# Kernel optimization log

Measured on AMD Instinct MI355X. Metric: run time of the kernel, lower is better.

Reference implementation:

```python
import jax, jax.numpy as jnp
import numpy as np

H_IMG, W_IMG = 224, 224  # image_size default in forward


def setup_inputs() -> dict:
    key = jax.random.key(0)
    k0, k1, k2 = jax.random.split(key, 3)
    B, C, M, N = 4, 256, 1024, 16384
    xyz_feats = jax.random.normal(k0, (B, C, M), jnp.float32)
    # projections land inside the image for a realistic bin distribution
    points = jax.random.uniform(k1, (B, N, 3), jnp.float32).at[..., 2].add(0.5)
    centers = jax.random.uniform(k2, (B, M, 3), jnp.float32).at[..., 2].add(0.5)
    fx = fy = 0.5 * W_IMG  # plausible intrinsics already scaled to 224x224
    K = jnp.array([[fx, 0.0, W_IMG / 2.0],
                   [0.0, fy, H_IMG / 2.0],
                   [0.0, 0.0, 1.0]], jnp.float32)
    return {"xyz_feats": xyz_feats, "points": points, "centers": centers,
            "K": K, "kernel_size": 4}


def reference(xyz_feats, points, centers, K, kernel_size):
    B, C, M = xyz_feats.shape
    N = points.shape[1]
    H, W = H_IMG, W_IMG

    # --- interpolating_points: PointNet++ 3-NN inverse-distance interp ---
    # squared pairwise distances [B, N, M]
    d2 = (jnp.sum(points * points, -1)[:, :, None]
          + jnp.sum(centers * centers, -1)[:, None, :]
          - 2.0 * jnp.einsum('bnd,bmd->bnm', points, centers))
    neg_d, idx = jax.lax.top_k(-d2, 3)            # 3 nearest centers, [B,N,3]
    w = 1.0 / (-neg_d + 1e-8)                     # inverse-distance weights
    w = w / jnp.sum(w, -1, keepdims=True)
    b3 = jnp.arange(B)[:, None, None]
    gathered = xyz_feats[b3, :, idx]              # [B, N, 3, C]
    interp = jnp.einsum('bnkc,bnk->bnc', gathered, w)  # [B, N, C]

    # --- project_to_image ---
    uvz = jnp.einsum('ij,bnj->bni', K, points)    # [B, N, 3]
    uv = uvz[..., :2] / jnp.maximum(uvz[..., 2:], 1e-8)
    u = jnp.clip(jnp.floor(uv[..., 0]), 0, W - 1).astype(jnp.int32)
    v = jnp.clip(jnp.floor(uv[..., 1]), 0, H - 1).astype(jnp.int32)
    idx_flat = u + v * W                          # [B, N]

    # --- scatter-add binning + count normalize ---
    bb = jnp.arange(B)[:, None]
    feat_map = jnp.zeros((B, H * W, C), interp.dtype).at[bb, idx_flat].add(interp)
    count = jnp.zeros((B, H * W), interp.dtype).at[bb, idx_flat].add(1.0)
    feat_map = feat_map / jnp.maximum(count, 1.0)[..., None]
    feat_map = feat_map.reshape(B, H, W, C).transpose(0, 3, 1, 2)  # [B,C,H,W]

    # --- avg_pool2d(kernel_size, stride=kernel_size) ---
    k = kernel_size
    out = feat_map.reshape(B, C, H // k, k, W // k, k).mean(axis=(3, 5))
    return out
```

## Files before the change

kernel.cpp:

```cpp
#include <hip/hip_runtime.h>
#include <hip/hip_bf16.h>

#define H_IMG 224
#define W_IMG 224
#define B_ 4
#define C_ 256
#define M_ 1024
#define N_ 16384
#define HW_ (H_IMG * W_IMG)
#define OH_ 56
#define OW_ 56
#define NBLK_ (OH_ * OW_)
#define NBINS_ (B_ * NBLK_)
#define NT_ (B_ * N_)
#define SEG_ 32
#define MAXSEG_ (NBINS_ + NT_ / SEG_)
#define KS_ 8
#define MC_ (M_ / KS_)
#define ZTOT_ (NBINS_ * C_ + B_ * HW_ + 2 * NBINS_ + 1)

__global__ __launch_bounds__(1024) void transpose_kernel(
    const float* __restrict__ xyz, float* __restrict__ XT,
    float* __restrict__ zeroRegion)
{
    __shared__ float tile[32][33];
    int b  = blockIdx.z;
    int c0 = blockIdx.x * 32;
    int m0 = blockIdx.y * 32;
    int tx = threadIdx.x, ty = threadIdx.y;
    int flat = ((blockIdx.z * gridDim.y + blockIdx.y) * gridDim.x + blockIdx.x)
               * 1024 + ty * 32 + tx;
    for (int i = flat; i < ZTOT_; i += 1024 * 1024) zeroRegion[i] = 0.0f;
    tile[ty][tx] = xyz[(b * C_ + c0 + ty) * M_ + m0 + tx];
    __syncthreads();
    XT[(b * M_ + m0 + ty) * C_ + c0 + tx] = tile[tx][ty];
}

__global__ __launch_bounds__(1024) void top3_kernel(
    const float* __restrict__ points, const float* __restrict__ centers,
    const float* __restrict__ Kmat,
    int* __restrict__ pixA, int* __restrict__ idA, float* __restrict__ wA,
    float* __restrict__ cnt, int* __restrict__ binCnt)
{
#pragma clang fp contract(off)
    __shared__ float4 cen[M_];
    __shared__ float  pd[KS_][256][3];
    __shared__ int    pi[KS_][256][3];
    int b  = blockIdx.y;
    int t  = threadIdx.x;
    int pl = t & 127;
    int s  = t >> 7;
    int nbase = blockIdx.x * 256;

    {
        float cx = centers[(b * M_ + t) * 3 + 0];
        float cy = centers[(b * M_ + t) * 3 + 1];
        float cz = centers[(b * M_ + t) * 3 + 2];
        float c2 = ((cx * cx) + (cy * cy)) + (cz * cz);
        cen[t] = make_float4(cx, cy, cz, c2);
    }
    __syncthreads();

    int nA = b * N_ + nbase + pl;
    int nB = nA + 128;
    float pxA = points[nA * 3 + 0], pyA = points[nA * 3 + 1], pzA = points[nA * 3 + 2];
    float pxB = points[nB * 3 + 0], pyB = points[nB * 3 + 1], pzB = points[nB * 3 + 2];
    float p2A = ((pxA * pxA) + (pyA * pyA)) + (pzA * pzA);
    float p2B = ((pxB * pxB) + (pyB * pyB)) + (pzB * pzB);

    float d0a = 1e30f, d1a = 1e30f, d2a = 1e30f;
    int   i0a = 0, i1a = 0, i2a = 0;
    float d0b = 1e30f, d1b = 1e30f, d2b = 1e30f;
    int   i0b = 0, i1b = 0, i2b = 0;
    int mbase = s * MC_;
#pragma unroll 2
    for (int j = 0; j < MC_; ++j) {
        int m = mbase + j;
        float4 cc = cen[m];
        float dotA = ((pzA * cc.z) + (pyA * cc.y)) + (pxA * cc.x);
        float dA   = (p2A + cc.w) - (2.0f * dotA);
        float dotB = ((pzB * cc.z) + (pyB * cc.y)) + (pxB * cc.x);
        float dB   = (p2B + cc.w) - (2.0f * dotB);
        if (dA < d2a) {
            if (dA < d1a) {
                d2a = d1a; i2a = i1a;
                if (dA < d0a) { d1a = d0a; i1a = i0a; d0a = dA; i0a = m; }
                else          { d1a = dA;  i1a = m; }
            } else { d2a = dA; i2a = m; }
        }
        if (dB < d2b) {
            if (dB < d1b) {
                d2b = d1b; i2b = i1b;
                if (dB < d0b) { d1b = d0b; i1b = i0b; d0b = dB; i0b = m; }
                else          { d1b = dB;  i1b = m; }
            } else { d2b = dB; i2b = m; }
        }
    }
    pd[s][pl][0] = d0a;  pd[s][pl][1] = d1a;  pd[s][pl][2] = d2a;
    pi[s][pl][0] = i0a;  pi[s][pl][1] = i1a;  pi[s][pl][2] = i2a;
    pd[s][pl + 128][0] = d0b;  pd[s][pl + 128][1] = d1b;  pd[s][pl + 128][2] = d2b;
    pi[s][pl + 128][0] = i0b;  pi[s][pl + 128][1] = i1b;  pi[s][pl + 128][2] = i2b;
    __syncthreads();

    if (t < 256) {
        float md0 = 1e30f, md1 = 1e30f, md2 = 1e30f;
        int   mi0 = M_,    mi1 = M_,    mi2 = M_;
#pragma unroll
        for (int ss = 0; ss < KS_; ++ss)
#pragma unroll
            for (int j = 0; j < 3; ++j) {
                float dd = pd[ss][t][j];
                int   ii = pi[ss][t][j];
                if ((dd < md2) || (dd == md2 && ii < mi2)) {
                    if ((dd < md1) || (dd == md1 && ii < mi1)) {
                        md2 = md1; mi2 = mi1;
                        if ((dd < md0) || (dd == md0 && ii < mi0)) {
                            md1 = md0; mi1 = mi0; md0 = dd; mi0 = ii;
                        } else { md1 = dd; mi1 = ii; }
                    } else { md2 = dd; mi2 = ii; }
                }
            }

        float w0 = 1.0f / (md0 + 1e-8f);
        float w1 = 1.0f / (md1 + 1e-8f);
        float w2 = 1.0f / (md2 + 1e-8f);
        float ws = (w0 + w1) + w2;
        w0 /= ws; w1 /= ws; w2 /= ws;

        int n = nbase + t;
        int g = b * N_ + n;
        float px = points[g * 3 + 0], py = points[g * 3 + 1], pz = points[g * 3 + 2];

        float fx = Kmat[0], cxk = Kmat[2], fy = Kmat[4], cyk = Kmat[5];
        float u_num = (cxk * pz) + (fx * px);
        float v_num = (cyk * pz) + (fy * py);
        float zc    = fmaxf(pz, 1e-8f);
        float u = floorf(u_num / zc);
        float v = floorf(v_num / zc);
        int ui = (int)fminf(fmaxf(u, 0.0f), (float)(W_IMG - 1));
        int vi = (int)fminf(fmaxf(v, 0.0f), (float)(H_IMG - 1));
        int pix = vi * W_IMG + ui;

        pixA[g] = pix;
        idA[g]           = mi0; idA[g + NT_]     = mi1; idA[g + 2 * NT_] = mi2;
        wA [g]           = w0;  wA [g + NT_]     = w1;  wA [g + 2 * NT_] = w2;
        atomicAdd(&cnt[b * HW_ + pix], 1.0f);
        int bin = b * NBLK_ + (vi >> 2) * OW_ + (ui >> 2);
        atomicAdd(&binCnt[bin], 1);
    }
}

__global__ __launch_bounds__(1024) void scan_kernel(
    const int* __restrict__ binCnt, int* __restrict__ binOff,
    int4* __restrict__ segs, int* __restrict__ segTotal)
{
    const int PER = (NBINS_ + 1023) / 1024;
    __shared__ int partK[1024], partS[1024];
    int t = threadIdx.x;
    int base = t * PER;
    int localK[PER], localS[PER];
    int sk = 0, sn = 0;
#pragma unroll
    for (int j = 0; j < PER; ++j) {
        int idx = base + j;
        int k  = (idx < NBINS_) ? binCnt[idx] : 0;
        int ns = 0;
        if (idx < NBINS_) { ns = (k + SEG_ - 1) / SEG_; if (ns == 0) ns = 1; }
        localK[j] = sk; localS[j] = sn;
        sk += k; sn += ns;
    }
    partK[t] = sk; partS[t] = sn;
    __syncthreads();
    for (int ofs = 1; ofs < 1024; ofs <<= 1) {
        int vK = (t >= ofs) ? partK[t - ofs] : 0;
        int vS = (t >= ofs) ? partS[t - ofs] : 0;
        __syncthreads();
        partK[t] += vK; partS[t] += vS;
        __syncthreads();
    }
    int exK = (t == 0) ? 0 : partK[t - 1];
    int exS = (t == 0) ? 0 : partS[t - 1];
#pragma unroll
    for (int j = 0; j < PER; ++j) {
        int idx = base + j;
        if (idx >= NBINS_) continue;
        int off = exK + localK[j];
        int sb  = exS + localS[j];
        binOff[idx] = off;
        int k = binCnt[idx];
        int nseg = (k + SEG_ - 1) / SEG_; if (nseg == 0) nseg = 1;
        for (int q = 0; q < nseg; ++q) {
            int len = k - q * SEG_;
            len = (len < 0) ? 0 : ((len > SEG_) ? SEG_ : len);
            segs[sb + q] = make_int4(idx, off + q * SEG_, len, nseg);
        }
    }
    if (t == 0) segTotal[0] = partS[1023];
}

__global__ __launch_bounds__(256) void pack_kernel(
    const int* __restrict__ pixA, const int* __restrict__ idA,
    const float* __restrict__ wA, const float* __restrict__ cnt,
    const int* __restrict__ binOff, int* __restrict__ binFill,
    int4* __restrict__ idP, float4* __restrict__ wP)
{
    int g = blockIdx.x * 256 + threadIdx.x;
    int b = g >> 14;
    int pix = pixA[g];
    int u = pix % W_IMG, v = pix / W_IMG;
    int bin = b * NBLK_ + (v >> 2) * OW_ + (u >> 2);
    int pos = atomicAdd(&binFill[bin], 1);
    int dst = binOff[bin] + pos;
    float s = 0.0625f / fmaxf(cnt[b * HW_ + pix], 1.0f);
    idP[dst] = make_int4(idA[g], idA[g + NT_], idA[g + 2 * NT_], b);
    wP[dst]  = make_float4(wA[g] * s, wA[g + NT_] * s, wA[g + 2 * NT_] * s, 0.0f);
}

__global__ __launch_bounds__(256) void gather_kernel(
    const float* __restrict__ XT, const int4* __restrict__ segs,
    const int* __restrict__ segTotal, const int4* __restrict__ idP,
    const float4* __restrict__ wP, float* __restrict__ tmp)
{
    int sid = blockIdx.x;
    if (sid >= segTotal[0]) return;
    int4 sg   = segs[sid];
    int bin   = sg.x, start = sg.y, len = sg.z, nseg = sg.w;
    int b     = bin / NBLK_;
    int c     = threadIdx.x;

    __shared__ int4   sId[SEG_];
    __shared__ float4 sW [SEG_];
    if (c < len) { sId[c] = idP[start + c]; sW[c] = wP[start + c]; }
    __syncthreads();

    const float* XTb = XT + (size_t)b * (M_ * C_);
    float acc = 0.0f;
    for (int j = 0; j < len; ++j) {
        int4   id = sId[j];
        float4 w  = sW[j];
        acc = fmaf(w.x, XTb[id.x * C_ + c],
              fmaf(w.y, XTb[id.y * C_ + c],
              fmaf(w.z, XTb[id.z * C_ + c], acc)));
    }

    float* dst = &tmp[(size_t)bin * C_ + c];
    if (nseg == 1) *dst = acc;
    else           atomicAdd(dst, acc);
}

__global__ __launch_bounds__(1024) void untranspose_kernel(
    const float* __restrict__ tmp, float* __restrict__ out)
{
    __shared__ float tile[32][33];
    int b  = blockIdx.z;
    int n0 = blockIdx.x * 32;
    int c0 = blockIdx.y * 32;
    int tx = threadIdx.x, ty = threadIdx.y;
    tile[ty][tx] = tmp[((size_t)b * NBLK_ + n0 + ty) * C_ + c0 + tx];
    __syncthreads();
    out[((size_t)(b * C_ + c0 + ty)) * NBLK_ + n0 + tx] = tile[tx][ty];
}

extern "C" void kernel_launch(void* const* d_in, const int* in_sizes, int n_in,
                              void* d_out, int out_size, void* d_ws, size_t ws_size,
                              hipStream_t stream)
{
    const float* xyz_feats = (const float*)d_in[0];
    const float* points    = (const float*)d_in[1];
    const float* centers   = (const float*)d_in[2];
    const float* Kmat      = (const float*)d_in[3];

    float* out = (float*)d_out;

    float*  XT       = (float*)d_ws;
    int4*   idP      = (int4*)(XT + (size_t)B_ * M_ * C_);
    float4* wP       = (float4*)(idP + NT_);
    int4*   segs     = (int4*)(wP + NT_);
    float*  tmp      = (float*)(segs + MAXSEG_);
    float*  cnt      = tmp + (size_t)NBINS_ * C_;
    int*    binCnt   = (int*)(cnt + (size_t)B_ * HW_);
    int*    binFill  = binCnt + NBINS_;
    int*    segTotal = binFill + NBINS_;
    int*    pixA     = segTotal + 1;
    int*    idA      = pixA + NT_;
    float*  wA       = (float*)(idA + 3 * NT_);
    int*    binOff   = (int*)(wA + 3 * NT_);

    dim3 tb(32, 32);
    dim3 tg(C_ / 32, M_ / 32, B_);
    transpose_kernel<<<tg, tb, 0, stream>>>(xyz_feats, XT, tmp);

    dim3 bg(N_ / 256, B_);
    top3_kernel<<<bg, 1024, 0, stream>>>(points, centers, Kmat,
                                         pixA, idA, wA, cnt, binCnt);

    scan_kernel<<<1, 1024, 0, stream>>>(binCnt, binOff, segs, segTotal);

    pack_kernel<<<NT_ / 256, 256, 0, stream>>>(pixA, idA, wA, cnt,
                                               binOff, binFill, idP, wP);

    gather_kernel<<<MAXSEG_, 256, 0, stream>>>(XT, segs, segTotal,
                                               idP, wP, tmp);

    dim3 ug(NBLK_ / 32, C_ / 32, B_);
    untranspose_kernel<<<ug, tb, 0, stream>>>(tmp, out);
}
```

Before: 187.5 us.

## Fuse all pipeline stages into one cooperative persistent kernel with grid syncs

```diff
diff --git a/kernel.cpp b/kernel.cpp
--- a/kernel.cpp
+++ b/kernel.cpp
@@ -1,5 +1,8 @@
 #include <hip/hip_runtime.h>
+#include <hip/hip_cooperative_groups.h>
 #include <hip/hip_bf16.h>
+
+namespace cg = cooperative_groups;
 
 #define H_IMG 224
 #define W_IMG 224
@@ -17,260 +20,259 @@
 #define MAXSEG_ (NBINS_ + NT_ / SEG_)
 #define KS_ 8
 #define MC_ (M_ / KS_)
+#define PTS_ 128
+#define NTILE3_ (B_ * N_ / PTS_)
 #define ZTOT_ (NBINS_ * C_ + B_ * HW_ + 2 * NBINS_ + 1)
-
-__global__ __launch_bounds__(1024) void transpose_kernel(
-    const float* __restrict__ xyz, float* __restrict__ XT,
-    float* __restrict__ zeroRegion)
-{
-    __shared__ float tile[32][33];
-    int b  = blockIdx.z;
-    int c0 = blockIdx.x * 32;
-    int m0 = blockIdx.y * 32;
-    int tx = threadIdx.x, ty = threadIdx.y;
-    int flat = ((blockIdx.z * gridDim.y + blockIdx.y) * gridDim.x + blockIdx.x)
-               * 1024 + ty * 32 + tx;
-    for (int i = flat; i < ZTOT_; i += 1024 * 1024) zeroRegion[i] = 0.0f;
-    tile[ty][tx] = xyz[(b * C_ + c0 + ty) * M_ + m0 + tx];
-    __syncthreads();
-    XT[(b * M_ + m0 + ty) * C_ + c0 + tx] = tile[tx][ty];
-}
-
-__global__ __launch_bounds__(1024) void top3_kernel(
-    const float* __restrict__ points, const float* __restrict__ centers,
-    const float* __restrict__ Kmat,
-    int* __restrict__ pixA, int* __restrict__ idA, float* __restrict__ wA,
-    float* __restrict__ cnt, int* __restrict__ binCnt)
+#define SCAN_PER_ ((NBINS_ + 1023) / 1024)
+
+struct Params {
+    const float* xyz; const float* points; const float* centers; const float* K;
+    float* out;
+    float* XT; int4* idP; float4* wP; int4* segs;
+    float* tmp; float* cnt; int* binCnt; int* binFill; int* segTotal;
+    int* pixA; int* idA; float* wA; int* binOff;
+    float* zeroRegion;
+};
+
+__global__ __launch_bounds__(1024, 8) void mega_kernel(Params P)
 {
 #pragma clang fp contract(off)
-    __shared__ float4 cen[M_];
-    __shared__ float  pd[KS_][256][3];
-    __shared__ int    pi[KS_][256][3];
-    int b  = blockIdx.y;
-    int t  = threadIdx.x;
-    int pl = t & 127;
-    int s  = t >> 7;
-    int nbase = blockIdx.x * 256;
+    cg::grid_group grd = cg::this_grid();
+    const int t   = threadIdx.x;
+    const int bid = blockIdx.x;
+    const int G   = gridDim.x;
+
+    __shared__ __attribute__((aligned(16))) char smraw[40960];
+    float  (*tile)[33] = reinterpret_cast<float (*)[33]>(smraw);
+    float4* cen  = reinterpret_cast<float4*>(smraw);
+    float*  pd   = reinterpret_cast<float*>(smraw + 16384);
+    int*    pi   = reinterpret_cast<int*>(smraw + 28672);
+    int*    partK= reinterpret_cast<int*>(smraw);
+    int*    partS= reinterpret_cast<int*>(smraw + 4096);
+    int4*   sIdA = reinterpret_cast<int4*>(smraw + 8192);
+    float4* sWA  = reinterpret_cast<float4*>(smraw + 8192 + 4 * SEG_ * 16);
 
     {
-        float cx = centers[(b * M_ + t) * 3 + 0];
-        float cy = centers[(b * M_ + t) * 3 + 1];
-        float cz = centers[(b * M_ + t) * 3 + 2];
-        float c2 = ((cx * cx) + (cy * cy)) + (cz * cz);
-        cen[t] = make_float4(cx, cy, cz, c2);
-    }
-    __syncthreads();
-
-    int nA = b * N_ + nbase + pl;
-    int nB = nA + 128;
-    float pxA = points[nA * 3 + 0], pyA = points[nA * 3 + 1], pzA = points[nA * 3 + 2];
-    float pxB = points[nB * 3 + 0], pyB = points[nB * 3 + 1], pzB = points[nB * 3 + 2];
-    float p2A = ((pxA * pxA) + (pyA * pyA)) + (pzA * pzA);
-    float p2B = ((pxB * pxB) + (pyB * pyB)) + (pzB * pzB);
-
-    float d0a = 1e30f, d1a = 1e30f, d2a = 1e30f;
-    int   i0a = 0, i1a = 0, i2a = 0;
-    float d0b = 1e30f, d1b = 1e30f, d2b = 1e30f;
-    int   i0b = 0, i1b = 0, i2b = 0;
-    int mbase = s * MC_;
-#pragma unroll 2
-    for (int j = 0; j < MC_; ++j) {
-        int m = mbase + j;
-        float4 cc = cen[m];
-        float dotA = ((pzA * cc.z) + (pyA * cc.y)) + (pxA * cc.x);
-        float dA   = (p2A + cc.w) - (2.0f * dotA);
-        float dotB = ((pzB * cc.z) + (pyB * cc.y)) + (pxB * cc.x);
-        float dB   = (p2B + cc.w) - (2.0f * dotB);
-        if (dA < d2a) {
-            if (dA < d1a) {
-                d2a = d1a; i2a = i1a;
-                if (dA < d0a) { d1a = d0a; i1a = i0a; d0a = dA; i0a = m; }
-                else          { d1a = dA;  i1a = m; }
-            } else { d2a = dA; i2a = m; }
-        }
-        if (dB < d2b) {
-            if (dB < d1b) {
-                d2b = d1b; i2b = i1b;
-                if (dB < d0b) { d1b = d0b; i1b = i0b; d0b = dB; i0b = m; }
-                else          { d1b = dB;  i1b = m; }
-            } else { d2b = dB; i2b = m; }
-        }
-    }
-    pd[s][pl][0] = d0a;  pd[s][pl][1] = d1a;  pd[s][pl][2] = d2a;
-    pi[s][pl][0] = i0a;  pi[s][pl][1] = i1a;  pi[s][pl][2] = i2a;
-    pd[s][pl + 128][0] = d0b;  pd[s][pl + 128][1] = d1b;  pd[s][pl + 128][2] = d2b;
-    pi[s][pl + 128][0] = i0b;  pi[s][pl + 128][1] = i1b;  pi[s][pl + 128][2] = i2b;
-    __syncthreads();
-
-    if (t < 256) {
-        float md0 = 1e30f, md1 = 1e30f, md2 = 1e30f;
-        int   mi0 = M_,    mi1 = M_,    mi2 = M_;
+        int gtid = bid * 1024 + t;
+        for (int i = gtid; i < ZTOT_; i += G * 1024) P.zeroRegion[i] = 0.0f;
+        int tx = t & 31, ty = t >> 5;
+        for (int tid2 = bid; tid2 < 1024; tid2 += G) {
+            int b  = tid2 >> 8;
+            int r  = tid2 & 255;
+            int c0 = (r >> 5) * 32;
+            int m0 = (r & 31) * 32;
+            __syncthreads();
+            tile[ty][tx] = P.xyz[(b * C_ + c0 + ty) * M_ + m0 + tx];
+            __syncthreads();
+            P.XT[(b * M_ + m0 + ty) * C_ + c0 + tx] = tile[tx][ty];
+        }
+    }
+    grd.sync();
+
+    for (int tid3 = bid; tid3 < NTILE3_; tid3 += G) {
+        int b     = tid3 >> 7;
+        int nbase = (tid3 & 127) * PTS_;
+        __syncthreads();
+        {
+            const float* cb = P.centers + (size_t)(b * M_ + t) * 3;
+            float cx = cb[0], cy = cb[1], cz = cb[2];
+            float c2 = ((cx * cx) + (cy * cy)) + (cz * cz);
+            cen[t] = make_float4(cx, cy, cz, c2);
+        }
+        __syncthreads();
+
+        int pl = t & 127;
+        int s  = t >> 7;
+        int g0 = b * N_ + nbase + pl;
+        const float* pp = P.points + (size_t)g0 * 3;
+        float px = pp[0], py = pp[1], pz = pp[2];
+        float p2 = ((px * px) + (py * py)) + (pz * pz);
+
+        float d0 = 1e30f, d1 = 1e30f, d2v = 1e30f;
+        int   i0 = 0, i1 = 0, i2 = 0;
+        int mbase = s * MC_;
+#pragma unroll 4
+        for (int j = 0; j < MC_; ++j) {
+            int m = mbase + j;
+            float4 cc = cen[m];
+            float dot = ((pz * cc.z) + (py * cc.y)) + (px * cc.x);
+            float d   = (p2 + cc.w) - (2.0f * dot);
+            if (d < d2v) {
+                if (d < d1) {
+                    d2v = d1; i2 = i1;
+                    if (d < d0) { d1 = d0; i1 = i0; d0 = d; i0 = m; }
+                    else        { d1 = d;  i1 = m; }
+                } else { d2v = d; i2 = m; }
+            }
+        }
+        int pb = (s * PTS_ + pl) * 3;
+        pd[pb] = d0;  pd[pb + 1] = d1;  pd[pb + 2] = d2v;
+        pi[pb] = i0;  pi[pb + 1] = i1;  pi[pb + 2] = i2;
+        __syncthreads();
+
+        if (t < PTS_) {
+            float md0 = 1e30f, md1 = 1e30f, md2 = 1e30f;
+            int   mi0 = M_,    mi1 = M_,    mi2 = M_;
 #pragma unroll
-        for (int ss = 0; ss < KS_; ++ss)
+            for (int ss = 0; ss < KS_; ++ss)
 #pragma unroll
-            for (int j = 0; j < 3; ++j) {
-                float dd = pd[ss][t][j];
-                int   ii = pi[ss][t][j];
-                if ((dd < md2) || (dd == md2 && ii < mi2)) {
-                    if ((dd < md1) || (dd == md1 && ii < mi1)) {
-                        md2 = md1; mi2 = mi1;
-                        if ((dd < md0) || (dd == md0 && ii < mi0)) {
-                            md1 = md0; mi1 = mi0; md0 = dd; mi0 = ii;
-                        } else { md1 = dd; mi1 = ii; }
-                    } else { md2 = dd; mi2 = ii; }
+                for (int j = 0; j < 3; ++j) {
+                    float dd = pd[(ss * PTS_ + t) * 3 + j];
+                    int   ii = pi[(ss * PTS_ + t) * 3 + j];
+                    if ((dd < md2) || (dd == md2 && ii < mi2)) {
+                        if ((dd < md1) || (dd == md1 && ii < mi1)) {
+                            md2 = md1; mi2 = mi1;
+                            if ((dd < md0) || (dd == md0 && ii < mi0)) {
+                                md1 = md0; mi1 = mi0; md0 = dd; mi0 = ii;
+                            } else { md1 = dd; mi1 = ii; }
+                        } else { md2 = dd; mi2 = ii; }
+                    }
                 }
+
+            float w0 = 1.0f / (md0 + 1e-8f);
+            float w1 = 1.0f / (md1 + 1e-8f);
+            float w2 = 1.0f / (md2 + 1e-8f);
+            float ws = (w0 + w1) + w2;
+            w0 /= ws; w1 /= ws; w2 /= ws;
+
+            int g = b * N_ + nbase + t;
+            const float* pq = P.points + (size_t)g * 3;
+            float qx = pq[0], qy = pq[1], qz = pq[2];
+            float fx = P.K[0], cxk = P.K[2], fy = P.K[4], cyk = P.K[5];
+            float u_num = (cxk * qz) + (fx * qx);
+            float v_num = (cyk * qz) + (fy * qy);
+            float zc    = fmaxf(qz, 1e-8f);
+            float u = floorf(u_num / zc);
+            float v = floorf(v_num / zc);
+            int ui = (int)fminf(fmaxf(u, 0.0f), (float)(W_IMG - 1));
+            int vi = (int)fminf(fmaxf(v, 0.0f), (float)(H_IMG - 1));
+            int pix = vi * W_IMG + ui;
+
+            P.pixA[g] = pix;
+            P.idA[g] = mi0; P.idA[g + NT_] = mi1; P.idA[g + 2 * NT_] = mi2;
+            P.wA [g] = w0;  P.wA [g + NT_] = w1;  P.wA [g + 2 * NT_] = w2;
+            atomicAdd(&P.cnt[b * HW_ + pix], 1.0f);
+            int bin = b * NBLK_ + (vi >> 2) * OW_ + (ui >> 2);
+            atomicAdd(&P.binCnt[bin], 1);
+        }
+    }
+    grd.sync();
+
+    if (bid == 0) {
+        int base = t * SCAN_PER_;
+        int localK[SCAN_PER_], localS[SCAN_PER_];
+        int sk = 0, sn = 0;
+#pragma unroll
+        for (int j = 0; j < SCAN_PER_; ++j) {
+            int idx = base + j;
+            int k = (idx < NBINS_) ? P.binCnt[idx] : 0;
+            int ns = 0;
+            if (idx < NBINS_) { ns = (k + SEG_ - 1) / SEG_; if (ns == 0) ns = 1; }
+            localK[j] = sk; localS[j] = sn;
+            sk += k; sn += ns;
+        }
+        partK[t] = sk; partS[t] = sn;
+        __syncthreads();
+        for (int ofs = 1; ofs < 1024; ofs <<= 1) {
+            int vK = (t >= ofs) ? partK[t - ofs] : 0;
+            int vS = (t >= ofs) ? partS[t - ofs] : 0;
+            __syncthreads();
+            partK[t] += vK; partS[t] += vS;
+            __syncthreads();
+        }
+        int exK = (t == 0) ? 0 : partK[t - 1];
+        int exS = (t == 0) ? 0 : partS[t - 1];
+#pragma unroll
+        for (int j = 0; j < SCAN_PER_; ++j) {
+            int idx = base + j;
+            if (idx >= NBINS_) continue;
+            int off = exK + localK[j];
+            int sb  = exS + localS[j];
+            P.binOff[idx] = off;
+            int k = P.binCnt[idx];
+            int nseg = (k + SEG_ - 1) / SEG_; if (nseg == 0) nseg = 1;
+            for (int q = 0; q < nseg; ++q) {
+                int len = k - q * SEG_;
+                len = (len < 0) ? 0 : ((len > SEG_) ? SEG_ : len);
+                P.segs[sb + q] = make_int4(idx, off + q * SEG_, len, nseg);
             }
-
-        float w0 = 1.0f / (md0 + 1e-8f);
-        float w1 = 1.0f / (md1 + 1e-8f);
-        float w2 = 1.0f / (md2 + 1e-8f);
-        float ws = (w0 + w1) + w2;
-        w0 /= ws; w1 /= ws; w2 /= ws;
-
-        int n = nbase + t;
-        int g = b * N_ + n;
-        float px = points[g * 3 + 0], py = points[g * 3 + 1], pz = points[g * 3 + 2];
-
-        float fx = Kmat[0], cxk = Kmat[2], fy = Kmat[4], cyk = Kmat[5];
-        float u_num = (cxk * pz) + (fx * px);
-        float v_num = (cyk * pz) + (fy * py);
-        float zc    = fmaxf(pz, 1e-8f);
-        float u = floorf(u_num / zc);
-        float v = floorf(v_num / zc);
-        int ui = (int)fminf(fmaxf(u, 0.0f), (float)(W_IMG - 1));
-        int vi = (int)fminf(fmaxf(v, 0.0f), (float)(H_IMG - 1));
-        int pix = vi * W_IMG + ui;
-
-        pixA[g] = pix;
-        idA[g]           = mi0; idA[g + NT_]     = mi1; idA[g + 2 * NT_] = mi2;
-        wA [g]           = w0;  wA [g + NT_]     = w1;  wA [g + 2 * NT_] = w2;
-        atomicAdd(&cnt[b * HW_ + pix], 1.0f);
-        int bin = b * NBLK_ + (vi >> 2) * OW_ + (ui >> 2);
-        atomicAdd(&binCnt[bin], 1);
-    }
-}
-
-__global__ __launch_bounds__(1024) void scan_kernel(
-    const int* __restrict__ binCnt, int* __restrict__ binOff,
-    int4* __restrict__ segs, int* __restrict__ segTotal)
-{
-    const int PER = (NBINS_ + 1023) / 1024;
-    __shared__ int partK[1024], partS[1024];
-    int t = threadIdx.x;
-    int base = t * PER;
-    int localK[PER], localS[PER];
-    int sk = 0, sn = 0;
-#pragma unroll
-    for (int j = 0; j < PER; ++j) {
-        int idx = base + j;
-        int k  = (idx < NBINS_) ? binCnt[idx] : 0;
-        int ns = 0;
-        if (idx < NBINS_) { ns = (k + SEG_ - 1) / SEG_; if (ns == 0) ns = 1; }
-        localK[j] = sk; localS[j] = sn;
-        sk += k; sn += ns;
-    }
-    partK[t] = sk; partS[t] = sn;
-    __syncthreads();
-    for (int ofs = 1; ofs < 1024; ofs <<= 1) {
-        int vK = (t >= ofs) ? partK[t - ofs] : 0;
-        int vS = (t >= ofs) ? partS[t - ofs] : 0;
-        __syncthreads();
-        partK[t] += vK; partS[t] += vS;
-        __syncthreads();
-    }
-    int exK = (t == 0) ? 0 : partK[t - 1];
-    int exS = (t == 0) ? 0 : partS[t - 1];
-#pragma unroll
-    for (int j = 0; j < PER; ++j) {
-        int idx = base + j;
-        if (idx >= NBINS_) continue;
-        int off = exK + localK[j];
-        int sb  = exS + localS[j];
-        binOff[idx] = off;
-        int k = binCnt[idx];
-        int nseg = (k + SEG_ - 1) / SEG_; if (nseg == 0) nseg = 1;
-        for (int q = 0; q < nseg; ++q) {
-            int len = k - q * SEG_;
-            len = (len < 0) ? 0 : ((len > SEG_) ? SEG_ : len);
-            segs[sb + q] = make_int4(idx, off + q * SEG_, len, nseg);
-        }
-    }
-    if (t == 0) segTotal[0] = partS[1023];
-}
-
-__global__ __launch_bounds__(256) void pack_kernel(
-    const int* __restrict__ pixA, const int* __restrict__ idA,
-    const float* __restrict__ wA, const float* __restrict__ cnt,
-    const int* __restrict__ binOff, int* __restrict__ binFill,
-    int4* __restrict__ idP, float4* __restrict__ wP)
-{
-    int g = blockIdx.x * 256 + threadIdx.x;
-    int b = g >> 14;
-    int pix = pixA[g];
-    int u = pix % W_IMG, v = pix / W_IMG;
-    int bin = b * NBLK_ + (v >> 2) * OW_ + (u >> 2);
-    int pos = atomicAdd(&binFill[bin], 1);
-    int dst = binOff[bin] + pos;
-    float s = 0.0625f / fmaxf(cnt[b * HW_ + pix], 1.0f);
-    idP[dst] = make_int4(idA[g], idA[g + NT_], idA[g + 2 * NT_], b);
-    wP[dst]  = make_float4(wA[g] * s, wA[g + NT_] * s, wA[g + 2 * NT_] * s, 0.0f);
-}
-
-__global__ __launch_bounds__(256) void gather_kernel(
-    const float* __restrict__ XT, const int4* __restrict__ segs,
-    const int* __restrict__ segTotal, const int4* __restrict__ idP,
-    const float4* __restrict__ wP, float* __restrict__ tmp)
-{
-    int sid = blockIdx.x;
-    if (sid >= segTotal[0]) return;
-    int4 sg   = segs[sid];
-    int bin   = sg.x, start = sg.y, len = sg.z, nseg = sg.w;
-    int b     = bin / NBLK_;
-    int c     = threadIdx.x;
-
-    __shared__ int4   sId[SEG_];
-    __shared__ float4 sW [SEG_];
-    if (c < len) { sId[c] = idP[start + c]; sW[c] = wP[start + c]; }
-    __syncthreads();
-
-    const float* XTb = XT + (size_t)b * (M_ * C_);
-    float acc = 0.0f;
-    for (int j = 0; j < len; ++j) {
-        int4   id = sId[j];
-        float4 w  = sW[j];
-        acc = fmaf(w.x, XTb[id.x * C_ + c],
-              fmaf(w.y, XTb[id.y * C_ + c],
-              fmaf(w.z, XTb[id.z * C_ + c], acc)));
-    }
-
-    float* dst = &tmp[(size_t)bin * C_ + c];
-    if (nseg == 1) *dst = acc;
-    else           atomicAdd(dst, acc);
-}
-
-__global__ __launch_bounds__(1024) void untranspose_kernel(
-    const float* __restrict__ tmp, float* __restrict__ out)
-{
-    __shared__ float tile[32][33];
-    int b  = blockIdx.z;
-    int n0 = blockIdx.x * 32;
-    int c0 = blockIdx.y * 32;
-    int tx = threadIdx.x, ty = threadIdx.y;
-    tile[ty][tx] = tmp[((size_t)b * NBLK_ + n0 + ty) * C_ + c0 + tx];
-    __syncthreads();
-    out[((size_t)(b * C_ + c0 + ty)) * NBLK_ + n0 + tx] = tile[tx][ty];
+        }
+        if (t == 0) P.segTotal[0] = partS[1023];
+    }
+    grd.sync();
+
+    for (int g = bid * 1024 + t; g < NT_; g += G * 1024) {
+        int b = g >> 14;
+        int pix = P.pixA[g];
+        int u = pix % W_IMG, v = pix / W_IMG;
+        int bin = b * NBLK_ + (v >> 2) * OW_ + (u >> 2);
+        int pos = atomicAdd(&P.binFill[bin], 1);
+        int dst = P.binOff[bin] + pos;
+        float sc = 0.0625f / fmaxf(P.cnt[b * HW_ + pix], 1.0f);
+        P.idP[dst] = make_int4(P.idA[g], P.idA[g + NT_], P.idA[g + 2 * NT_], b);
+        P.wP[dst]  = make_float4(P.wA[g] * sc, P.wA[g + NT_] * sc,
+                                 P.wA[g + 2 * NT_] * sc, 0.0f);
+    }
+    grd.sync();
+
+    {
+        int segTot = P.segTotal[0];
+        int sub = t >> 8, c = t & 255;
+        int4*   mysId = sIdA + sub * SEG_;
+        float4* mysW  = sWA  + sub * SEG_;
+        for (int base2 = bid * 4; base2 < segTot; base2 += G * 4) {
+            int sid = base2 + sub;
+            bool active = (sid < segTot);
+            int4 sg = make_int4(0, 0, 0, 1);
+            if (active) sg = P.segs[sid];
+            __syncthreads();
+            if (active && c < sg.z) { mysId[c] = P.idP[sg.y + c];
+                                      mysW[c]  = P.wP[sg.y + c]; }
+            __syncthreads();
+            if (active) {
+                int bin = sg.x;
+                int b = bin / NBLK_;
+                const float* XTb = P.XT + (size_t)b * (M_ * C_);
+                float acc = 0.0f;
+                for (int j = 0; j < sg.z; ++j) {
+                    int4 id = mysId[j]; float4 w = mysW[j];
+                    acc = fmaf(w.x, XTb[id.x * C_ + c],
+                          fmaf(w.y, XTb[id.y * C_ + c],
+                          fmaf(w.z, XTb[id.z * C_ + c], acc)));
+                }
+                float* dst = &P.tmp[(size_t)bin * C_ + c];
+                if (sg.w == 1) *dst = acc;
+                else           atomicAdd(dst, acc);
+            }
+        }
+    }
+    grd.sync();
+
+    {
+        int tx = t & 31, ty = t >> 5;
+        for (int tid6 = bid; tid6 < 3136; tid6 += G) {
+            int b  = tid6 / 784;
+            int r  = tid6 - b * 784;
+            int c0 = (r & 7) * 32;
+            int n0 = (r >> 3) * 32;
+            __syncthreads();
+            tile[ty][tx] = P.tmp[((size_t)b * NBLK_ + n0 + ty) * C_ + c0 + tx];
+            __syncthreads();
+            P.out[((size_t)(b * C_ + c0 + ty)) * NBLK_ + n0 + tx] = tile[tx][ty];
+        }
+    }
 }
 
 extern "C" void kernel_launch(void* const* d_in, const int* in_sizes, int n_in,
                               void* d_out, int out_size, void* d_ws, size_t ws_size,
                               hipStream_t stream)
 {
-    const float* xyz_feats = (const float*)d_in[0];
-    const float* points    = (const float*)d_in[1];
-    const float* centers   = (const float*)d_in[2];
-    const float* Kmat      = (const float*)d_in[3];
-
-    float* out = (float*)d_out;
+    Params P;
+    P.xyz     = (const float*)d_in[0];
+    P.points  = (const float*)d_in[1];
+    P.centers = (const float*)d_in[2];
+    P.K       = (const float*)d_in[3];
+    P.out     = (float*)d_out;
 
     float*  XT       = (float*)d_ws;
     int4*   idP      = (int4*)(XT + (size_t)B_ * M_ * C_);
@@ -286,22 +288,19 @@
     float*  wA       = (float*)(idA + 3 * NT_);
     int*    binOff   = (int*)(wA + 3 * NT_);
 
-    dim3 tb(32, 32);
-    dim3 tg(C_ / 32, M_ / 32, B_);
-    transpose_kernel<<<tg, tb, 0, stream>>>(xyz_feats, XT, tmp);
-
-    dim3 bg(N_ / 256, B_);
-    top3_kernel<<<bg, 1024, 0, stream>>>(points, centers, Kmat,
-                                         pixA, idA, wA, cnt, binCnt);
-
-    scan_kernel<<<1, 1024, 0, stream>>>(binCnt, binOff, segs, segTotal);
-
-    pack_kernel<<<NT_ / 256, 256, 0, stream>>>(pixA, idA, wA, cnt,
-                                               binOff, binFill, idP, wP);
-
-    gather_kernel<<<MAXSEG_, 256, 0, stream>>>(XT, segs, segTotal,
-                                               idP, wP, tmp);
-
-    dim3 ug(NBLK_ / 32, C_ / 32, B_);
-    untranspose_kernel<<<ug, tb, 0, stream>>>(tmp, out);
+    P.XT = XT; P.idP = idP; P.wP = wP; P.segs = segs; P.tmp = tmp;
+    P.cnt = cnt; P.binCnt = binCnt; P.binFill = binFill; P.segTotal = segTotal;
+    P.pixA = pixA; P.idA = idA; P.wA = wA; P.binOff = binOff;
+    P.zeroRegion = tmp;
+
+    int maxB = 0;
+    if (hipOccupancyMaxActiveBlocksPerMultiprocessor(
+            &maxB, reinterpret_cast<const void*>(mega_kernel), 1024, 0)
+        != hipSuccess || maxB < 1) maxB = 1;
+    int G = maxB * 256;
+    if (G > NTILE3_) G = NTILE3_;
+
+    void* kargs[] = { &P };
+    hipLaunchCooperativeKernel(reinterpret_cast<const void*>(mega_kernel),
+                               dim3(G), dim3(1024), kargs, 0, stream);
 }
```

Measured after the change: 347.6 us. 85.4% more time.

## Branchless top-3 insertion, one point per thread, dual accumulators in gather

Applied to the files above, without the earlier changes.

```diff
diff --git a/kernel.cpp b/kernel.cpp
--- a/kernel.cpp
+++ b/kernel.cpp
@@ -17,6 +17,7 @@
 #define MAXSEG_ (NBINS_ + NT_ / SEG_)
 #define KS_ 8
 #define MC_ (M_ / KS_)
+#define PTS_ 128
 #define ZTOT_ (NBINS_ * C_ + B_ * HW_ + 2 * NBINS_ + 1)
 
 __global__ __launch_bounds__(1024) void transpose_kernel(
@@ -36,7 +37,7 @@
     XT[(b * M_ + m0 + ty) * C_ + c0 + tx] = tile[tx][ty];
 }
 
-__global__ __launch_bounds__(1024) void top3_kernel(
+__global__ __launch_bounds__(1024, 8) void top3_kernel(
     const float* __restrict__ points, const float* __restrict__ centers,
     const float* __restrict__ Kmat,
     int* __restrict__ pixA, int* __restrict__ idA, float* __restrict__ wA,
@@ -44,65 +45,55 @@
 {
 #pragma clang fp contract(off)
     __shared__ float4 cen[M_];
-    __shared__ float  pd[KS_][256][3];
-    __shared__ int    pi[KS_][256][3];
-    int b  = blockIdx.y;
-    int t  = threadIdx.x;
-    int pl = t & 127;
-    int s  = t >> 7;
-    int nbase = blockIdx.x * 256;
+    __shared__ float  pd[KS_][PTS_][3];
+    __shared__ int    pi[KS_][PTS_][3];
+    int b     = blockIdx.y;
+    int t     = threadIdx.x;
+    int pl    = t & 127;
+    int s     = t >> 7;
+    int nbase = blockIdx.x * PTS_;
 
     {
-        float cx = centers[(b * M_ + t) * 3 + 0];
-        float cy = centers[(b * M_ + t) * 3 + 1];
-        float cz = centers[(b * M_ + t) * 3 + 2];
+        const float* cb = centers + (size_t)(b * M_ + t) * 3;
+        float cx = cb[0], cy = cb[1], cz = cb[2];
         float c2 = ((cx * cx) + (cy * cy)) + (cz * cz);
         cen[t] = make_float4(cx, cy, cz, c2);
     }
     __syncthreads();
 
-    int nA = b * N_ + nbase + pl;
-    int nB = nA + 128;
-    float pxA = points[nA * 3 + 0], pyA = points[nA * 3 + 1], pzA = points[nA * 3 + 2];
-    float pxB = points[nB * 3 + 0], pyB = points[nB * 3 + 1], pzB = points[nB * 3 + 2];
-    float p2A = ((pxA * pxA) + (pyA * pyA)) + (pzA * pzA);
-    float p2B = ((pxB * pxB) + (pyB * pyB)) + (pzB * pzB);
-
-    float d0a = 1e30f, d1a = 1e30f, d2a = 1e30f;
-    int   i0a = 0, i1a = 0, i2a = 0;
-    float d0b = 1e30f, d1b = 1e30f, d2b = 1e30f;
-    int   i0b = 0, i1b = 0, i2b = 0;
+    int g0 = b * N_ + nbase + pl;
+    const float* pp = points + (size_t)g0 * 3;
+    float px = pp[0], py = pp[1], pz = pp[2];
+    float p2 = ((px * px) + (py * py)) + (pz * pz);
+
+    float d0 = 1e30f, d1 = 1e30f, d2v = 1e30f;
+    int   i0 = 0, i1 = 0, i2 = 0;
     int mbase = s * MC_;
-#pragma unroll 2
+#pragma unroll 4
     for (int j = 0; j < MC_; ++j) {
         int m = mbase + j;
         float4 cc = cen[m];
-        float dotA = ((pzA * cc.z) + (pyA * cc.y)) + (pxA * cc.x);
-        float dA   = (p2A + cc.w) - (2.0f * dotA);
-        float dotB = ((pzB * cc.z) + (pyB * cc.y)) + (pxB * cc.x);
-        float dB   = (p2B + cc.w) - (2.0f * dotB);
-        if (dA < d2a) {
-            if (dA < d1a) {
-                d2a = d1a; i2a = i1a;
-                if (dA < d0a) { d1a = d0a; i1a = i0a; d0a = dA; i0a = m; }
-                else          { d1a = dA;  i1a = m; }
-            } else { d2a = dA; i2a = m; }
-        }
-        if (dB < d2b) {
-            if (dB < d1b) {
-                d2b = d1b; i2b = i1b;
-                if (dB < d0b) { d1b = d0b; i1b = i0b; d0b = dB; i0b = m; }
-                else          { d1b = dB;  i1b = m; }
-            } else { d2b = dB; i2b = m; }
-        }
-    }
-    pd[s][pl][0] = d0a;  pd[s][pl][1] = d1a;  pd[s][pl][2] = d2a;
-    pi[s][pl][0] = i0a;  pi[s][pl][1] = i1a;  pi[s][pl][2] = i2a;
-    pd[s][pl + 128][0] = d0b;  pd[s][pl + 128][1] = d1b;  pd[s][pl + 128][2] = d2b;
-    pi[s][pl + 128][0] = i0b;  pi[s][pl + 128][1] = i1b;  pi[s][pl + 128][2] = i2b;
-    __syncthreads();
-
-    if (t < 256) {
+        float dot = ((pz * cc.z) + (py * cc.y)) + (px * cc.x);
+        float d   = (p2 + cc.w) - (2.0f * dot);
+        bool  c0  = d < d0;
+        float l0  = fmaxf(d, d0);
+        int   li0 = c0 ? i0 : m;
+        d0 = fminf(d, d0);
+        i0 = c0 ? m : i0;
+        bool  c1  = l0 < d1;
+        float l1  = fmaxf(l0, d1);
+        int   li1 = c1 ? i1 : li0;
+        d1 = fminf(l0, d1);
+        i1 = c1 ? li0 : i1;
+        bool  c2  = l1 < d2v;
+        d2v = fminf(l1, d2v);
+        i2  = c2 ? li1 : i2;
+    }
+    pd[s][pl][0] = d0;  pd[s][pl][1] = d1;  pd[s][pl][2] = d2v;
+    pi[s][pl][0] = i0;  pi[s][pl][1] = i1;  pi[s][pl][2] = i2;
+    __syncthreads();
+
+    if (t < PTS_) {
         float md0 = 1e30f, md1 = 1e30f, md2 = 1e30f;
         int   mi0 = M_,    mi1 = M_,    mi2 = M_;
 #pragma unroll
@@ -127,14 +118,13 @@
         float ws = (w0 + w1) + w2;
         w0 /= ws; w1 /= ws; w2 /= ws;
 
-        int n = nbase + t;
-        int g = b * N_ + n;
-        float px = points[g * 3 + 0], py = points[g * 3 + 1], pz = points[g * 3 + 2];
-
+        int g = b * N_ + nbase + t;
+        const float* pq = points + (size_t)g * 3;
+        float qx = pq[0], qy = pq[1], qz = pq[2];
         float fx = Kmat[0], cxk = Kmat[2], fy = Kmat[4], cyk = Kmat[5];
-        float u_num = (cxk * pz) + (fx * px);
-        float v_num = (cyk * pz) + (fy * py);
-        float zc    = fmaxf(pz, 1e-8f);
+        float u_num = (cxk * qz) + (fx * qx);
+        float v_num = (cyk * qz) + (fy * qy);
+        float zc    = fmaxf(qz, 1e-8f);
         float u = floorf(u_num / zc);
         float v = floorf(v_num / zc);
         int ui = (int)fminf(fmaxf(u, 0.0f), (float)(W_IMG - 1));
@@ -234,14 +224,25 @@
     __syncthreads();
 
     const float* XTb = XT + (size_t)b * (M_ * C_);
-    float acc = 0.0f;
-    for (int j = 0; j < len; ++j) {
-        int4   id = sId[j];
-        float4 w  = sW[j];
-        acc = fmaf(w.x, XTb[id.x * C_ + c],
-              fmaf(w.y, XTb[id.y * C_ + c],
-              fmaf(w.z, XTb[id.z * C_ + c], acc)));
-    }
+    float accA = 0.0f, accB = 0.0f;
+    int j = 0;
+    for (; j + 1 < len; j += 2) {
+        int4 ia = sId[j];     float4 wa = sW[j];
+        int4 ib = sId[j + 1]; float4 wb = sW[j + 1];
+        accA = fmaf(wa.x, XTb[ia.x * C_ + c],
+               fmaf(wa.y, XTb[ia.y * C_ + c],
+               fmaf(wa.z, XTb[ia.z * C_ + c], accA)));
+        accB = fmaf(wb.x, XTb[ib.x * C_ + c],
+               fmaf(wb.y, XTb[ib.y * C_ + c],
+               fmaf(wb.z, XTb[ib.z * C_ + c], accB)));
+    }
+    if (j < len) {
+        int4 ia = sId[j]; float4 wa = sW[j];
+        accA = fmaf(wa.x, XTb[ia.x * C_ + c],
+               fmaf(wa.y, XTb[ia.y * C_ + c],
+               fmaf(wa.z, XTb[ia.z * C_ + c], accA)));
+    }
+    float acc = accA + accB;
 
     float* dst = &tmp[(size_t)bin * C_ + c];
     if (nseg == 1) *dst = acc;
@@ -290,7 +291,7 @@
     dim3 tg(C_ / 32, M_ / 32, B_);
     transpose_kernel<<<tg, tb, 0, stream>>>(xyz_feats, XT, tmp);
 
-    dim3 bg(N_ / 256, B_);
+    dim3 bg(N_ / PTS_, B_);
     top3_kernel<<<bg, 1024, 0, stream>>>(points, centers, Kmat,
                                          pixA, idA, wA, cnt, binCnt);
 
```

Result: no change. 186.9 us (-0.3%).
